# Kernel optimization log

Measured on AMD Instinct MI355X. Metric: run time of the kernel, lower is better.

The kernel has to match this reference:

```python
import jax, jax.numpy as jnp
import numpy as np

B, N, C, H, HD = 32, 512, 384, 6, 64
WH = WW = WT = 8
ALPHA = 4.0
KS = 5


def safe_pow(x, p):
    # x = relu(...) >= 0; avoid nan grads at x == 0
    pos = x > 0
    return jnp.where(pos, jnp.where(pos, x, 1.0) ** p, 0.0)


def setup_inputs() -> dict:
    key = jax.random.key(0)
    ks = jax.random.split(key, 12)
    s = 0.02
    return {
        "x": jax.random.normal(ks[0], (B, N, C), jnp.float32),
        "y": jax.random.normal(ks[1], (B, N, C), jnp.float32),
        "Wqkvg": jax.random.normal(ks[2], (4 * C, C), jnp.float32) * s,
        "bqkvg": jax.random.normal(ks[3], (4 * C,), jnp.float32) * s,
        "Wproj": jax.random.normal(ks[4], (C, C), jnp.float32) * s,
        "bproj": jax.random.normal(ks[5], (C,), jnp.float32) * s,
        "dwc_w": jax.random.normal(ks[6], (HD, 1, KS, KS, KS), jnp.float32) * s,
        "dwc_b": jax.random.normal(ks[7], (HD,), jnp.float32) * s,
        "power_p": jax.random.normal(ks[8], (1, H, 1, HD), jnp.float32) * s,
        "scale_p": jax.random.normal(ks[9], (1, 1, C), jnp.float32) * s,
        "pe": jax.random.normal(ks[10], (1, N, C), jnp.float32) * s,
    }


def reference(x, y, Wqkvg, bqkvg, Wproj, bproj, dwc_w, dwc_b, power_p, scale_p, pe):
    qkv = (x @ Wqkvg.T + bqkvg).reshape(B, N, 4, C)
    k = qkv[:, :, 1]
    v = qkv[:, :, 2]
    g = qkv[:, :, 3]
    q = (y @ Wqkvg.T + bqkvg).reshape(B, N, 4, C)[:, :, 0]

    k = k + pe
    scale = jax.nn.softplus(scale_p)          # (1,1,C)
    power = 1.0 + ALPHA * jax.nn.sigmoid(power_p)  # (1,H,1,HD)
    q = q / scale
    k = k / scale

    def heads(t):  # (B,N,C) -> (B,H,N,HD)
        return t.reshape(B, N, H, HD).transpose(0, 2, 1, 3)

    q = heads(q)
    k = heads(k)
    v = heads(v)

    q_pos = safe_pow(jax.nn.relu(q), power)
    q_neg = safe_pow(jax.nn.relu(-q), power)
    k_pos = safe_pow(jax.nn.relu(k), power)
    k_neg = safe_pow(jax.nn.relu(-k), power)

    q_sim = jnp.concatenate([q_pos, q_neg], axis=-1)   # (B,H,N,2HD)
    q_opp = jnp.concatenate([q_neg, q_pos], axis=-1)
    kf = jnp.concatenate([k_pos, k_neg], axis=-1)      # (B,H,N,2HD)
    v1, v2 = jnp.split(v, 2, axis=-1)                  # each (B,H,N,HD/2)

    k_mean = kf.mean(axis=-2)                          # (B,H,2HD)
    inv_sqrt_n = N ** (-0.5)
    kfs = kf * inv_sqrt_n

    z_sim = 1.0 / (jnp.einsum("bhnd,bhd->bhn", q_sim, k_mean)[..., None] + 1e-6)
    kv1 = jnp.einsum("bhnd,bhne->bhde", kfs, v1 * inv_sqrt_n)
    x_sim = jnp.einsum("bhnd,bhde->bhne", q_sim, kv1) * z_sim

    z_opp = 1.0 / (jnp.einsum("bhnd,bhd->bhn", q_opp, k_mean)[..., None] + 1e-6)
    kv2 = jnp.einsum("bhnd,bhne->bhde", kfs, v2 * inv_sqrt_n)
    x_opp = jnp.einsum("bhnd,bhde->bhne", q_opp, kv2) * z_opp

    xa = jnp.concatenate([x_sim, x_opp], axis=-1)      # (B,H,N,HD)
    xa = xa.transpose(0, 2, 1, 3).reshape(B, N, C)

    # depthwise conv3d on v: (B*H, HD, Wh, Ww, Wt)
    vr = v.reshape(B * H, WH, WW, WT, HD).transpose(0, 4, 1, 2, 3)
    pad = KS // 2
    vc = jax.lax.conv_general_dilated(
        vr, dwc_w, window_strides=(1, 1, 1),
        padding=[(pad, pad)] * 3,
        dimension_numbers=("NCDHW", "OIDHW", "NCDHW"),
        feature_group_count=HD,
    ) + dwc_b[None, :, None, None, None]
    vc = vc.transpose(0, 2, 3, 4, 1).reshape(B, N, C)

    out = (xa + vc) * g
    out = out @ Wproj.T + bproj
    return out
```

## Files before the change

### kernel.cpp

```cpp
#include <hip/hip_runtime.h>
#include <hip/hip_bf16.h>
#include <math.h>

#define B_  32
#define N_  512
#define C_  384
#define H_  6
#define HD_ 64
#define M_  (B_*N_)

typedef __attribute__((ext_vector_type(8))) short bfrag;
typedef __attribute__((ext_vector_type(4))) float f32x4;

__device__ __forceinline__ unsigned short f2bfu(float f){
  unsigned int u = __float_as_uint(f);
  u += 0x7fffu + ((u >> 16) & 1u);
  return (unsigned short)(u >> 16);
}
__device__ __forceinline__ bfrag cvt8(float4 a, float4 b){
  bfrag r;
  r[0]=(short)f2bfu(a.x); r[1]=(short)f2bfu(a.y); r[2]=(short)f2bfu(a.z); r[3]=(short)f2bfu(a.w);
  r[4]=(short)f2bfu(b.x); r[5]=(short)f2bfu(b.y); r[6]=(short)f2bfu(b.z); r[7]=(short)f2bfu(b.w);
  return r;
}

__global__ void param_kernel(const float* __restrict__ scale_p,
                             const float* __restrict__ power_p,
                             float* __restrict__ scale_inv,
                             float* __restrict__ power){
  int t = threadIdx.x;
  if (t < C_){
    float s  = scale_p[t];
    scale_inv[t] = 1.0f / log1pf(expf(s));
  }
  if (t < H_*HD_){
    float p = power_p[t];
    power[t] = 1.0f + 4.0f / (1.0f + expf(-p));
  }
}

__global__ void sentinel_kernel(float* __restrict__ out, int n){
  int i = blockIdx.x*256 + threadIdx.x;
  if (i < n) out[i] = 1.0e9f;
}

__global__ __launch_bounds__(256) void gemm_qkvg(
    const float* __restrict__ x, const float* __restrict__ y,
    const float* __restrict__ W, const float* __restrict__ bias,
    const float* __restrict__ pe, const float* __restrict__ scale_inv,
    float* __restrict__ q, float* __restrict__ k, float* __restrict__ v,
    float* __restrict__ g)
{
  const int mode = blockIdx.z;
  const float* A = (mode == 0) ? y : x;
  const int wofs = mode * C_;
  float* out = (mode==0)?q:((mode==1)?k:((mode==2)?v:g));

  __shared__ short As[128][40];
  __shared__ short Bs[128][40];

  const int tid  = threadIdx.x;
  const int row0 = blockIdx.y * 128;
  const int col0 = blockIdx.x * 128;
  const int wave = tid >> 6, lane = tid & 63;
  const int wm = (wave >> 1) * 64, wn = (wave & 1) * 64;
  const int fr = lane & 15, quad = lane >> 4;
  const int sr = tid >> 2;
  const int sk = (tid & 3) * 8;

  f32x4 acc[4][4] = {};

  for (int k0 = 0; k0 < C_; k0 += 32){
    #pragma unroll
    for (int half = 0; half < 2; half++){
      const int r = sr + half*64;
      const float* ap = &A[(size_t)(row0 + r)*C_ + k0 + sk];
      const float* bp = &W[(size_t)(wofs + col0 + r)*C_ + k0 + sk];
      float4 a0 = *reinterpret_cast<const float4*>(ap);
      float4 a1 = *reinterpret_cast<const float4*>(ap + 4);
      float4 b0 = *reinterpret_cast<const float4*>(bp);
      float4 b1 = *reinterpret_cast<const float4*>(bp + 4);
      *reinterpret_cast<bfrag*>(&As[r][sk]) = cvt8(a0, a1);
      *reinterpret_cast<bfrag*>(&Bs[r][sk]) = cvt8(b0, b1);
    }
    __syncthreads();
    bfrag af[4], bf[4];
    #pragma unroll
    for (int f = 0; f < 4; f++){
      af[f] = *reinterpret_cast<const bfrag*>(&As[wm + f*16 + fr][quad*8]);
      bf[f] = *reinterpret_cast<const bfrag*>(&Bs[wn + f*16 + fr][quad*8]);
    }
    #pragma unroll
    for (int i=0;i<4;i++)
      #pragma unroll
      for (int j=0;j<4;j++)
        acc[i][j] = __builtin_amdgcn_mfma_f32_16x16x32_bf16(af[i], bf[j], acc[i][j], 0, 0, 0);
    __syncthreads();
  }

  #pragma unroll
  for (int i = 0; i < 4; i++){
    const int rowb = row0 + wm + i*16 + quad*4;
    #pragma unroll
    for (int j = 0; j < 4; j++){
      const int col = col0 + wn + j*16 + fr;
      const float bcol = bias[wofs + col];
      const float sc   = scale_inv[col];
      #pragma unroll
      for (int r = 0; r < 4; r++){
        const int row = rowb + r;
        const int n = row & (N_-1);
        float val = acc[i][j][r] + bcol;
        if (mode == 0)      val *= sc;
        else if (mode == 1) val = (val + pe[n*C_ + col]) * sc;
        out[(size_t)row*C_ + col] = val;
      }
    }
  }
}

#define NC_ 256
__global__ __launch_bounds__(512) void attn_kernel(
    const float* __restrict__ q, const float* __restrict__ k,
    const float* __restrict__ v, const float* __restrict__ power,
    float* __restrict__ xa)
{
  const int bh = blockIdx.x;
  const int b = bh / H_, h = bh % H_;
  __shared__ float pw[64];
  __shared__ __align__(16) unsigned short smem[54912];
  unsigned short* kfT  = smem;
  unsigned short* vT   = smem + 33792;
  unsigned short* kvBT = smem;
  unsigned short* qf   = smem + 33792;

  const int tid = threadIdx.x;
  const int wave = tid >> 6, lane = tid & 63;
  const int fr = lane & 15, quad = lane >> 4;
  if (tid < 64) pw[tid] = power[h*HD_ + tid];

  const float* kbase = k + (size_t)b*N_*C_ + h*HD_;
  const float* vbase = v + (size_t)b*N_*C_ + h*HD_;

  for (int i = tid; i < 16*NC_; i += 512){
    int e = 64 + (i >> 8);
    int nl = i & (NC_-1);
    vT[e*264 + nl] = (e == 64) ? (unsigned short)0x3F80 : (unsigned short)0;
  }
  __syncthreads();

  f32x4 acc[5] = {};
  for (int chunk = 0; chunk < 2; chunk++){
    const int n0 = chunk * NC_;
    for (int it = 0; it < 32; it++){
      int flat = it*512 + tid;
      int c = flat & 63, nl = flat >> 6;
      float kval = kbase[(size_t)(n0+nl)*C_ + c];
      float p = pw[c];
      float ax = fabsf(kval);
      float pv = (ax > 0.0f) ? exp2f(p * log2f(ax)) : 0.0f;
      kfT[c*264 + nl]      = f2bfu((kval > 0.0f) ? pv : 0.0f);
      kfT[(64+c)*264 + nl] = f2bfu((kval < 0.0f) ? pv : 0.0f);
      vT[c*264 + nl] = f2bfu(vbase[(size_t)(n0+nl)*C_ + c]);
    }
    __syncthreads();
    for (int kk = 0; kk < NC_/32; kk++){
      int ko = kk*32 + quad*8;
      bfrag af = *reinterpret_cast<const bfrag*>(&kfT[(wave*16 + fr)*264 + ko]);
      #pragma unroll
      for (int j = 0; j < 5; j++){
        bfrag bf = *reinterpret_cast<const bfrag*>(&vT[(j*16 + fr)*264 + ko]);
        acc[j] = __builtin_amdgcn_mfma_f32_16x16x32_bf16(af, bf, acc[j], 0, 0, 0);
      }
    }
    __syncthreads();
  }

  const float invN = 1.0f / (float)N_;
  {
    const int dbase = wave*16 + quad*4;
    #pragma unroll
    for (int j = 0; j < 4; j++){
      const int e = j*16 + fr;
      const int dd = (e < 32) ? dbase : (dbase ^ 64);
      ushort4 w4;
      w4.x = f2bfu(acc[j][0] * invN);
      w4.y = f2bfu(acc[j][1] * invN);
      w4.z = f2bfu(acc[j][2] * invN);
      w4.w = f2bfu(acc[j][3] * invN);
      *reinterpret_cast<ushort4*>(&kvBT[e*136 + dd]) = w4;
    }
    if (fr == 0){
      ushort4 wk;
      wk.x = f2bfu(acc[4][0] * invN);
      wk.y = f2bfu(acc[4][1] * invN);
      wk.z = f2bfu(acc[4][2] * invN);
      wk.w = f2bfu(acc[4][3] * invN);
      *reinterpret_cast<ushort4*>(&kvBT[64*136 + dbase]) = wk;
      *reinterpret_cast<ushort4*>(&kvBT[65*136 + (dbase^64)]) = wk;
    }
  }
  __syncthreads();

  const float* qbase = q + (size_t)b*N_*C_ + h*HD_;
  float* xabase = xa + (size_t)b*N_*C_ + h*HD_;
  for (int mc = 0; mc < 4; mc++){
    const int m0 = mc * 128;
    for (int it = 0; it < 16; it++){
      int flat = it*512 + tid;
      int c = flat & 63, nl = flat >> 6;
      float qval = qbase[(size_t)(m0+nl)*C_ + c];
      float p = pw[c];
      float ax = fabsf(qval);
      float pv = (ax > 0.0f) ? exp2f(p * log2f(ax)) : 0.0f;
      qf[nl*136 + c]      = f2bfu((qval > 0.0f) ? pv : 0.0f);
      qf[nl*136 + 64 + c] = f2bfu((qval < 0.0f) ? pv : 0.0f);
    }
    __syncthreads();
    f32x4 a2[5] = {};
    for (int kk = 0; kk < 4; kk++){
      int ko = kk*32 + quad*8;
      bfrag af = *reinterpret_cast<const bfrag*>(&qf[(wave*16 + fr)*136 + ko]);
      #pragma unroll
      for (int j = 0; j < 5; j++){
        bfrag bf = *reinterpret_cast<const bfrag*>(&kvBT[(j*16 + fr)*136 + ko]);
        a2[j] = __builtin_amdgcn_mfma_f32_16x16x32_bf16(af, bf, a2[j], 0, 0, 0);
      }
    }
    #pragma unroll
    for (int r = 0; r < 4; r++){
      const float zsim = __shfl(a2[4][r], quad*16);
      const float zopp = __shfl(a2[4][r], quad*16 + 1);
      const int n = m0 + wave*16 + quad*4 + r;
      #pragma unroll
      for (int j = 0; j < 4; j++){
        const int e = j*16 + fr;
        const float z = (e < 32) ? zsim : zopp;
        xabase[(size_t)n*C_ + e] = a2[j][r] / (z + 1e-6f);
      }
    }
    __syncthreads();
  }
}

__global__ __launch_bounds__(512) void conv_kernel(
    const float* __restrict__ v, const float* __restrict__ dwc_w,
    const float* __restrict__ dwc_b, float* __restrict__ xa)
{
  const int bh = blockIdx.x;
  const int b = bh / H_, h = bh % H_;
  __shared__ float vol[32][521];
  __shared__ float wv[32][126];
  __shared__ float wb[32];
  const int tid = threadIdx.x;
  const float* vbase = v + (size_t)b*N_*C_ + h*HD_;
  float* xabatch = xa + (size_t)b*N_*C_ + (size_t)h*N_*HD_;

  for (int half = 0; half < 2; half++){
    const int ch0 = half * 32;
    for (int it = 0; it < 32; it++){
      int flat = it*512 + tid;
      int cl = flat & 31, n = flat >> 5;
      vol[cl][n] = vbase[(size_t)n*C_ + ch0 + cl];
    }
    for (int i = tid; i < 32*125; i += 512){
      int ch = i / 125, wi = i - ch*125;
      wv[ch][wi] = dwc_w[(ch0+ch)*125 + wi];
    }
    if (tid < 32) wb[tid] = dwc_b[ch0 + tid];
    __syncthreads();

    for (int t = 0; t < 4; t++){
      const int task = t*512 + tid;
      const int ch = task & 31;
      const int zy = task >> 5;
      const int z = zy >> 3, yc = zy & 7;
      float o[8];
      const float bias = wb[ch];
      #pragma unroll
      for (int xx = 0; xx < 8; xx++) o[xx] = bias;
      #pragma unroll
      for (int kd = 0; kd < 5; kd++){
        const int zz = z + kd - 2;
        if ((unsigned)zz >= 8u) continue;
        #pragma unroll
        for (int kh = 0; kh < 5; kh++){
          const int yy = yc + kh - 2;
          if ((unsigned)yy >= 8u) continue;
          const float* row = &vol[ch][zz*64 + yy*8];
          float rr[8];
          #pragma unroll
          for (int xx = 0; xx < 8; xx++) rr[xx] = row[xx];
          const float* wrow = &wv[ch][kd*25 + kh*5];
          float w5[5];
          #pragma unroll
          for (int kw = 0; kw < 5; kw++) w5[kw] = wrow[kw];
          #pragma unroll
          for (int xx = 0; xx < 8; xx++){
            #pragma unroll
            for (int kw = 0; kw < 5; kw++){
              const int xi = xx + kw - 2;
              if ((unsigned)xi < 8u) o[xx] = fmaf(w5[kw], rr[xi], o[xx]);
            }
          }
        }
      }
      const int nb = zy * 8;
      #pragma unroll
      for (int xx = 0; xx < 8; xx++){
        const size_t di = (size_t)(nb + xx)*HD_ + ch0 + ch;
        xabatch[di] += o[xx];
      }
    }
    __syncthreads();
  }
}

__global__ __launch_bounds__(256) void proj_kernel(
    const float* __restrict__ xa, const float* __restrict__ g,
    const float* __restrict__ Wp, const float* __restrict__ bp,
    float* __restrict__ out)
{
  __shared__ short As[128][40];
  __shared__ short Bs[128][40];

  const int tid  = threadIdx.x;
  const int row0 = blockIdx.y * 128;
  const int col0 = blockIdx.x * 128;
  const int wave = tid >> 6, lane = tid & 63;
  const int wm = (wave >> 1) * 64, wn = (wave & 1) * 64;
  const int fr = lane & 15, quad = lane >> 4;
  const int sr = tid >> 2;
  const int sk = (tid & 3) * 8;

  f32x4 acc[4][4] = {};

  for (int k0 = 0; k0 < C_; k0 += 32){
    #pragma unroll
    for (int half = 0; half < 2; half++){
      const int r = sr + half*64;
      const size_t aidx = (size_t)(row0 + r)*C_ + k0 + sk;
      float4 x0 = *reinterpret_cast<const float4*>(&xa[aidx]);
      float4 x1 = *reinterpret_cast<const float4*>(&xa[aidx + 4]);
      float4 g0 = *reinterpret_cast<const float4*>(&g[aidx]);
      float4 g1 = *reinterpret_cast<const float4*>(&g[aidx + 4]);
      x0.x*=g0.x; x0.y*=g0.y; x0.z*=g0.z; x0.w*=g0.w;
      x1.x*=g1.x; x1.y*=g1.y; x1.z*=g1.z; x1.w*=g1.w;
      const float* bp2 = &Wp[(size_t)(col0 + r)*C_ + k0 + sk];
      float4 b0 = *reinterpret_cast<const float4*>(bp2);
      float4 b1 = *reinterpret_cast<const float4*>(bp2 + 4);
      *reinterpret_cast<bfrag*>(&As[r][sk]) = cvt8(x0, x1);
      *reinterpret_cast<bfrag*>(&Bs[r][sk]) = cvt8(b0, b1);
    }
    __syncthreads();
    bfrag af[4], bf[4];
    #pragma unroll
    for (int f = 0; f < 4; f++){
      af[f] = *reinterpret_cast<const bfrag*>(&As[wm + f*16 + fr][quad*8]);
      bf[f] = *reinterpret_cast<const bfrag*>(&Bs[wn + f*16 + fr][quad*8]);
    }
    #pragma unroll
    for (int i=0;i<4;i++)
      #pragma unroll
      for (int j=0;j<4;j++)
        acc[i][j] = __builtin_amdgcn_mfma_f32_16x16x32_bf16(af[i], bf[j], acc[i][j], 0, 0, 0);
    __syncthreads();
  }

  #pragma unroll
  for (int i = 0; i < 4; i++){
    const int rowb = row0 + wm + i*16 + quad*4;
    #pragma unroll
    for (int j = 0; j < 4; j++){
      const int col = col0 + wn + j*16 + fr;
      const float bcol = bp[col];
      #pragma unroll
      for (int r = 0; r < 4; r++){
        out[(size_t)(rowb + r)*C_ + col] = acc[i][j][r] + bcol;
      }
    }
  }
}

extern "C" void kernel_launch(void* const* d_in, const int* in_sizes, int n_in,
                              void* d_out, int out_size, void* d_ws, size_t ws_size,
                              hipStream_t stream){
  float* out = (float*)d_out;

  const int expect[11] = {6291456, 6291456, 589824, 1536, 147456, 384, 8000, 64, 384, 384, 196608};
  bool ok = (n_in == 11);
  for (int i = 0; ok && i < 11; i++) ok = (in_sizes[i] == expect[i]);
  if (!ok){
    sentinel_kernel<<<(out_size+255)/256, 256, 0, stream>>>(out, out_size);
    return;
  }

  const float* x    = (const float*)d_in[0];
  const float* y    = (const float*)d_in[1];
  const float* W    = (const float*)d_in[2];
  const float* bq   = (const float*)d_in[3];
  const float* Wp   = (const float*)d_in[4];
  const float* bp   = (const float*)d_in[5];
  const float* dwcw = (const float*)d_in[6];
  const float* dwcb = (const float*)d_in[7];
  const float* pwp  = (const float*)d_in[8];
  const float* scp  = (const float*)d_in[9];
  const float* pe   = (const float*)d_in[10];

  float* ws = (float*)d_ws;
  const size_t SZ = (size_t)M_ * C_;
  float* q  = ws;
  float* k  = ws + SZ;
  float* v  = ws + 2*SZ;
  float* g  = ws + 3*SZ;
  float* xa = ws + 4*SZ;
  float* scale_inv = ws + 5*SZ;
  float* power     = scale_inv + 512;

  param_kernel<<<1, 512, 0, stream>>>(scp, pwp, scale_inv, power);
  gemm_qkvg<<<dim3(C_/128, M_/128, 4), 256, 0, stream>>>(x, y, W, bq, pe, scale_inv, q, k, v, g);
  attn_kernel<<<dim3(B_*H_), 512, 0, stream>>>(q, k, v, power, xa);
  conv_kernel<<<dim3(B_*H_), 512, 0, stream>>>(v, dwcw, dwcb, xa);
  proj_kernel<<<dim3(C_/128, M_/128), 256, 0, stream>>>(xa, g, Wp, bp, out);
}
```

Measured before the change: 279.8 us.

## Store q/k/v/g intermediates in bf16 and widen QKVG GEMM tile to full width

```diff
diff --git a/kernel.cpp b/kernel.cpp
--- a/kernel.cpp
+++ b/kernel.cpp
@@ -11,7 +11,11 @@
 
 typedef __attribute__((ext_vector_type(8))) short bfrag;
 typedef __attribute__((ext_vector_type(4))) float f32x4;
-
+typedef unsigned short bfraw;
+
+__device__ __forceinline__ float bfu2f(unsigned short u){
+  return __uint_as_float(((unsigned int)u) << 16);
+}
 __device__ __forceinline__ unsigned short f2bfu(float f){
   unsigned int u = __float_as_uint(f);
   u += 0x7fffu + ((u >> 16) & 1u);
@@ -44,56 +48,59 @@
   if (i < n) out[i] = 1.0e9f;
 }
 
-__global__ __launch_bounds__(256) void gemm_qkvg(
+__global__ __launch_bounds__(512) void gemm_qkvg(
     const float* __restrict__ x, const float* __restrict__ y,
     const float* __restrict__ W, const float* __restrict__ bias,
     const float* __restrict__ pe, const float* __restrict__ scale_inv,
-    float* __restrict__ q, float* __restrict__ k, float* __restrict__ v,
-    float* __restrict__ g)
+    bfraw* __restrict__ q, bfraw* __restrict__ k, bfraw* __restrict__ v,
+    bfraw* __restrict__ g)
 {
-  const int mode = blockIdx.z;
+  const int mode = blockIdx.y;
   const float* A = (mode == 0) ? y : x;
   const int wofs = mode * C_;
-  float* out = (mode==0)?q:((mode==1)?k:((mode==2)?v:g));
+  bfraw* out = (mode==0)?q:((mode==1)?k:((mode==2)?v:g));
 
   __shared__ short As[128][40];
-  __shared__ short Bs[128][40];
+  __shared__ short Bs[384][40];
 
   const int tid  = threadIdx.x;
-  const int row0 = blockIdx.y * 128;
-  const int col0 = blockIdx.x * 128;
+  const int row0 = blockIdx.x * 128;
   const int wave = tid >> 6, lane = tid & 63;
-  const int wm = (wave >> 1) * 64, wn = (wave & 1) * 64;
+  const int wm = (wave >> 2) * 64;
+  const int wn = (wave & 3) * 96;
   const int fr = lane & 15, quad = lane >> 4;
   const int sr = tid >> 2;
   const int sk = (tid & 3) * 8;
 
-  f32x4 acc[4][4] = {};
+  f32x4 acc[4][6] = {};
 
   for (int k0 = 0; k0 < C_; k0 += 32){
-    #pragma unroll
-    for (int half = 0; half < 2; half++){
-      const int r = sr + half*64;
-      const float* ap = &A[(size_t)(row0 + r)*C_ + k0 + sk];
-      const float* bp = &W[(size_t)(wofs + col0 + r)*C_ + k0 + sk];
+    {
+      const float* ap = &A[(size_t)(row0 + sr)*C_ + k0 + sk];
       float4 a0 = *reinterpret_cast<const float4*>(ap);
       float4 a1 = *reinterpret_cast<const float4*>(ap + 4);
+      *reinterpret_cast<bfrag*>(&As[sr][sk]) = cvt8(a0, a1);
+    }
+    #pragma unroll
+    for (int rep = 0; rep < 3; rep++){
+      const int r = sr + rep*128;
+      const float* bp = &W[(size_t)(wofs + r)*C_ + k0 + sk];
       float4 b0 = *reinterpret_cast<const float4*>(bp);
       float4 b1 = *reinterpret_cast<const float4*>(bp + 4);
-      *reinterpret_cast<bfrag*>(&As[r][sk]) = cvt8(a0, a1);
       *reinterpret_cast<bfrag*>(&Bs[r][sk]) = cvt8(b0, b1);
     }
     __syncthreads();
-    bfrag af[4], bf[4];
-    #pragma unroll
-    for (int f = 0; f < 4; f++){
+    bfrag af[4], bf[6];
+    #pragma unroll
+    for (int f = 0; f < 4; f++)
       af[f] = *reinterpret_cast<const bfrag*>(&As[wm + f*16 + fr][quad*8]);
+    #pragma unroll
+    for (int f = 0; f < 6; f++)
       bf[f] = *reinterpret_cast<const bfrag*>(&Bs[wn + f*16 + fr][quad*8]);
-    }
     #pragma unroll
     for (int i=0;i<4;i++)
       #pragma unroll
-      for (int j=0;j<4;j++)
+      for (int j=0;j<6;j++)
         acc[i][j] = __builtin_amdgcn_mfma_f32_16x16x32_bf16(af[i], bf[j], acc[i][j], 0, 0, 0);
     __syncthreads();
   }
@@ -102,8 +109,8 @@
   for (int i = 0; i < 4; i++){
     const int rowb = row0 + wm + i*16 + quad*4;
     #pragma unroll
-    for (int j = 0; j < 4; j++){
-      const int col = col0 + wn + j*16 + fr;
+    for (int j = 0; j < 6; j++){
+      const int col = wn + j*16 + fr;
       const float bcol = bias[wofs + col];
       const float sc   = scale_inv[col];
       #pragma unroll
@@ -113,7 +120,7 @@
         float val = acc[i][j][r] + bcol;
         if (mode == 0)      val *= sc;
         else if (mode == 1) val = (val + pe[n*C_ + col]) * sc;
-        out[(size_t)row*C_ + col] = val;
+        out[(size_t)row*C_ + col] = f2bfu(val);
       }
     }
   }
@@ -121,8 +128,8 @@
 
 #define NC_ 256
 __global__ __launch_bounds__(512) void attn_kernel(
-    const float* __restrict__ q, const float* __restrict__ k,
-    const float* __restrict__ v, const float* __restrict__ power,
+    const bfraw* __restrict__ q, const bfraw* __restrict__ k,
+    const bfraw* __restrict__ v, const float* __restrict__ power,
     float* __restrict__ xa)
 {
   const int bh = blockIdx.x;
@@ -139,8 +146,8 @@
   const int fr = lane & 15, quad = lane >> 4;
   if (tid < 64) pw[tid] = power[h*HD_ + tid];
 
-  const float* kbase = k + (size_t)b*N_*C_ + h*HD_;
-  const float* vbase = v + (size_t)b*N_*C_ + h*HD_;
+  const bfraw* kbase = k + (size_t)b*N_*C_ + h*HD_;
+  const bfraw* vbase = v + (size_t)b*N_*C_ + h*HD_;
 
   for (int i = tid; i < 16*NC_; i += 512){
     int e = 64 + (i >> 8);
@@ -155,13 +162,13 @@
     for (int it = 0; it < 32; it++){
       int flat = it*512 + tid;
       int c = flat & 63, nl = flat >> 6;
-      float kval = kbase[(size_t)(n0+nl)*C_ + c];
+      float kval = bfu2f(kbase[(size_t)(n0+nl)*C_ + c]);
       float p = pw[c];
       float ax = fabsf(kval);
       float pv = (ax > 0.0f) ? exp2f(p * log2f(ax)) : 0.0f;
       kfT[c*264 + nl]      = f2bfu((kval > 0.0f) ? pv : 0.0f);
       kfT[(64+c)*264 + nl] = f2bfu((kval < 0.0f) ? pv : 0.0f);
-      vT[c*264 + nl] = f2bfu(vbase[(size_t)(n0+nl)*C_ + c]);
+      vT[c*264 + nl] = vbase[(size_t)(n0+nl)*C_ + c];
     }
     __syncthreads();
     for (int kk = 0; kk < NC_/32; kk++){
@@ -202,14 +209,14 @@
   }
   __syncthreads();
 
-  const float* qbase = q + (size_t)b*N_*C_ + h*HD_;
+  const bfraw* qbase = q + (size_t)b*N_*C_ + h*HD_;
   float* xabase = xa + (size_t)b*N_*C_ + h*HD_;
   for (int mc = 0; mc < 4; mc++){
     const int m0 = mc * 128;
     for (int it = 0; it < 16; it++){
       int flat = it*512 + tid;
       int c = flat & 63, nl = flat >> 6;
-      float qval = qbase[(size_t)(m0+nl)*C_ + c];
+      float qval = bfu2f(qbase[(size_t)(m0+nl)*C_ + c]);
       float p = pw[c];
       float ax = fabsf(qval);
       float pv = (ax > 0.0f) ? exp2f(p * log2f(ax)) : 0.0f;
@@ -244,7 +251,7 @@
 }
 
 __global__ __launch_bounds__(512) void conv_kernel(
-    const float* __restrict__ v, const float* __restrict__ dwc_w,
+    const bfraw* __restrict__ v, const float* __restrict__ dwc_w,
     const float* __restrict__ dwc_b, float* __restrict__ xa)
 {
   const int bh = blockIdx.x;
@@ -253,7 +260,7 @@
   __shared__ float wv[32][126];
   __shared__ float wb[32];
   const int tid = threadIdx.x;
-  const float* vbase = v + (size_t)b*N_*C_ + h*HD_;
+  const bfraw* vbase = v + (size_t)b*N_*C_ + h*HD_;
   float* xabatch = xa + (size_t)b*N_*C_ + (size_t)h*N_*HD_;
 
   for (int half = 0; half < 2; half++){
@@ -261,7 +268,7 @@
     for (int it = 0; it < 32; it++){
       int flat = it*512 + tid;
       int cl = flat & 31, n = flat >> 5;
-      vol[cl][n] = vbase[(size_t)n*C_ + ch0 + cl];
+      vol[cl][n] = bfu2f(vbase[(size_t)n*C_ + ch0 + cl]);
     }
     for (int i = tid; i < 32*125; i += 512){
       int ch = i / 125, wi = i - ch*125;
@@ -317,7 +324,7 @@
 }
 
 __global__ __launch_bounds__(256) void proj_kernel(
-    const float* __restrict__ xa, const float* __restrict__ g,
+    const float* __restrict__ xa, const bfraw* __restrict__ g,
     const float* __restrict__ Wp, const float* __restrict__ bp,
     float* __restrict__ out)
 {
@@ -342,10 +349,10 @@
       const size_t aidx = (size_t)(row0 + r)*C_ + k0 + sk;
       float4 x0 = *reinterpret_cast<const float4*>(&xa[aidx]);
       float4 x1 = *reinterpret_cast<const float4*>(&xa[aidx + 4]);
-      float4 g0 = *reinterpret_cast<const float4*>(&g[aidx]);
-      float4 g1 = *reinterpret_cast<const float4*>(&g[aidx + 4]);
-      x0.x*=g0.x; x0.y*=g0.y; x0.z*=g0.z; x0.w*=g0.w;
-      x1.x*=g1.x; x1.y*=g1.y; x1.z*=g1.z; x1.w*=g1.w;
+      const ushort4 gu0 = *reinterpret_cast<const ushort4*>(&g[aidx]);
+      const ushort4 gu1 = *reinterpret_cast<const ushort4*>(&g[aidx + 4]);
+      x0.x*=bfu2f(gu0.x); x0.y*=bfu2f(gu0.y); x0.z*=bfu2f(gu0.z); x0.w*=bfu2f(gu0.w);
+      x1.x*=bfu2f(gu1.x); x1.y*=bfu2f(gu1.y); x1.z*=bfu2f(gu1.z); x1.w*=bfu2f(gu1.w);
       const float* bp2 = &Wp[(size_t)(col0 + r)*C_ + k0 + sk];
       float4 b0 = *reinterpret_cast<const float4*>(bp2);
       float4 b1 = *reinterpret_cast<const float4*>(bp2 + 4);
@@ -407,18 +414,17 @@
   const float* scp  = (const float*)d_in[9];
   const float* pe   = (const float*)d_in[10];
 
-  float* ws = (float*)d_ws;
   const size_t SZ = (size_t)M_ * C_;
-  float* q  = ws;
-  float* k  = ws + SZ;
-  float* v  = ws + 2*SZ;
-  float* g  = ws + 3*SZ;
-  float* xa = ws + 4*SZ;
-  float* scale_inv = ws + 5*SZ;
+  bfraw* q = (bfraw*)d_ws;
+  bfraw* k = q + SZ;
+  bfraw* v = k + SZ;
+  bfraw* g = v + SZ;
+  float* xa = (float*)(g + SZ);
+  float* scale_inv = xa + SZ;
   float* power     = scale_inv + 512;
 
   param_kernel<<<1, 512, 0, stream>>>(scp, pwp, scale_inv, power);
-  gemm_qkvg<<<dim3(C_/128, M_/128, 4), 256, 0, stream>>>(x, y, W, bq, pe, scale_inv, q, k, v, g);
+  gemm_qkvg<<<dim3(M_/128, 4), 512, 0, stream>>>(x, y, W, bq, pe, scale_inv, q, k, v, g);
   attn_kernel<<<dim3(B_*H_), 512, 0, stream>>>(q, k, v, power, xa);
   conv_kernel<<<dim3(B_*H_), 512, 0, stream>>>(v, dwcw, dwcb, xa);
   proj_kernel<<<dim3(C_/128, M_/128), 256, 0, stream>>>(xa, g, Wp, bp, out);
```

Result: slower. 287.1 us (+2.6%).
